# Kernel tuning notes

Hardware: AMD Instinct MI355X
Metric: run time of the kernel (lower is better)

Reference implementation:

```python
import jax, jax.numpy as jnp
import numpy as np

D_IN = 1024
D_OUT = 1024
NUM_HEADS = 16
HEAD_DIM = D_OUT // NUM_HEADS
EPS = 1e-6
POW = 16.0


def setup_inputs() -> dict:
    key = jax.random.key(0)
    ks = jax.random.split(key, 6)
    s = 1.0 / np.sqrt(D_IN)
    x = jax.random.normal(ks[0], (2, 2048, D_IN), dtype=jnp.float32)
    Wq = jax.random.uniform(ks[1], (D_OUT, D_IN), jnp.float32, -s, s)
    Wk = jax.random.uniform(ks[2], (D_OUT, D_IN), jnp.float32, -s, s)
    Wv = jax.random.uniform(ks[3], (D_OUT, D_IN), jnp.float32, -s, s)
    Wo = jax.random.uniform(ks[4], (D_OUT, D_OUT), jnp.float32, -s, s)
    bo = jax.random.uniform(ks[5], (D_OUT,), jnp.float32, -s, s)
    return {"x": x, "Wq": Wq, "Wk": Wk, "Wv": Wv, "Wo": Wo, "bo": bo}


def _l2norm(t):
    # torch F.normalize: t / max(||t||, eps)
    n = jnp.sqrt(jnp.sum(t * t, axis=-1, keepdims=True))
    return t / jnp.maximum(n, EPS)


def reference(x, Wq, Wk, Wv, Wo, bo):
    B, T, _ = x.shape
    # project and split heads: [B, H, T, Dh]
    def heads(W):
        y = jnp.einsum('btd,od->bto', x, W)
        return y.reshape(B, T, NUM_HEADS, HEAD_DIM).transpose(0, 2, 1, 3)
    Q = _l2norm(heads(Wq))
    K = _l2norm(heads(Wk))
    V = heads(Wv)
    cos_sim = jnp.clip(jnp.einsum('bhtd,bhsd->bhts', Q, K), -0.999, 0.999)
    scores = 1.0 - jnp.arccos(cos_sim) / jnp.pi
    W = jnp.power(jnp.maximum(scores, EPS), POW)
    W = W / (jnp.sum(W, axis=-1, keepdims=True) + EPS)
    out = jnp.einsum('bhts,bhsd->bhtd', W, V)
    out = out.transpose(0, 2, 1, 3).reshape(B, T, D_OUT)
    return jnp.einsum('bto,po->btp', out, Wo) + bo
```

## Files before the change

### kernel.cpp

```cpp
#include <hip/hip_runtime.h>
#include <math.h>

constexpr int Dm   = 1024;
constexpr int NH   = 16;
constexpr int HD   = 64;
constexpr int Bb   = 2;
constexpr int Tt   = 2048;
constexpr int MTOT = Bb * Tt;
#define EPSF 1e-6f

typedef __attribute__((ext_vector_type(8))) short short8;
typedef __attribute__((ext_vector_type(4))) float f32x4;
typedef __attribute__((ext_vector_type(2))) float f32x2;

__device__ __forceinline__ ushort f2bf(float f) {
    union { float f; unsigned u; } v; v.f = f;
    unsigned r = (v.u + 0x7FFFu + ((v.u >> 16) & 1u)) >> 16;
    return (ushort)r;
}

__device__ __forceinline__ void gload16(const void* g, void* l) {
    __builtin_amdgcn_global_load_lds(
        (const __attribute__((address_space(1))) unsigned int*)g,
        (__attribute__((address_space(3))) unsigned int*)l,
        16, 0, 0);
}

__global__ __launch_bounds__(256)
void cvt_all(const float* __restrict__ x,  const float* __restrict__ wq,
             const float* __restrict__ wk, const float* __restrict__ wv,
             const float* __restrict__ wo,
             ushort* __restrict__ xb,  ushort* __restrict__ wqb,
             ushort* __restrict__ wkb, ushort* __restrict__ wvb,
             ushort* __restrict__ wob) {
    int i = blockIdx.x * 256 + threadIdx.x;
    const float* src; ushort* dst; int off;
    if (i < 1048576)      { src = x;  dst = xb;  off = i; }
    else if (i < 1310720) { src = wq; dst = wqb; off = i - 1048576; }
    else if (i < 1572864) { src = wk; dst = wkb; off = i - 1310720; }
    else if (i < 1835008) { src = wv; dst = wvb; off = i - 1572864; }
    else                  { src = wo; dst = wob; off = i - 1835008; }
    const float4 v = ((const float4*)src)[off];
    ushort4 o;
    o.x = f2bf(v.x); o.y = f2bf(v.y); o.z = f2bf(v.z); o.w = f2bf(v.w);
    ((ushort4*)dst)[off] = o;
}

template<bool OUTF32>
__device__ __forceinline__
void gemm_core(const ushort* __restrict__ A, const ushort* __restrict__ W,
               const float* __restrict__ bias, void* __restrict__ out,
               int m0, int n0, int N, int K, int mode) {
    __shared__ ushort As[128 * 64];
    __shared__ ushort Bs[128 * 64];
    const int tid  = threadIdx.x;
    const int wave = tid >> 6, lane = tid & 63;
    const int quad = lane >> 4, l15 = lane & 15;
    const int wr = wave >> 1, wc = wave & 1;
    const int lr = lane >> 3;
    const int sc = (lane & 7) ^ lr;

    f32x4 acc[4][4] = {};
    const ushort* Ab = A + (size_t)(m0 + lr) * K + sc * 8;
    const ushort* Wb = W + (size_t)(n0 + lr) * K + sc * 8;

    for (int k0 = 0; k0 < K; k0 += 64) {
        #pragma unroll
        for (int i = 0; i < 4; i++) {
            const int rows8 = (wave * 4 + i) * 8;
            gload16(Ab + (size_t)rows8 * K + k0, &As[rows8 * 64]);
            gload16(Wb + (size_t)rows8 * K + k0, &Bs[rows8 * 64]);
        }
        __syncthreads();
        #pragma unroll
        for (int kh = 0; kh < 2; kh++) {
            short8 af[4];
            #pragma unroll
            for (int mi = 0; mi < 4; mi++) {
                const int row = wr * 64 + mi * 16 + l15;
                af[mi] = *(const short8*)&As[row * 64 + (((kh * 4 + quad) ^ (row & 7)) * 8)];
            }
            #pragma unroll
            for (int nj = 0; nj < 4; nj++) {
                const int row = wc * 64 + nj * 16 + l15;
                const short8 bf = *(const short8*)&Bs[row * 64 + (((kh * 4 + quad) ^ (row & 7)) * 8)];
                #pragma unroll
                for (int mi = 0; mi < 4; mi++)
                    acc[mi][nj] = __builtin_amdgcn_mfma_f32_16x16x32_bf16(af[mi], bf, acc[mi][nj], 0, 0, 0);
            }
        }
        __syncthreads();
    }

    if (!OUTF32 && mode == 2) {
        #pragma unroll
        for (int mi = 0; mi < 4; mi++) {
            const int t  = m0 + wr * 64 + mi * 16 + quad * 4;
            const int bb = t >> 11, tl = t & 2047;
            #pragma unroll
            for (int nj = 0; nj < 4; nj++) {
                const int n = n0 + wc * 64 + nj * 16 + l15;
                const int hh = n >> 6, dd = n & 63;
                uint2 pk;
                pk.x = (unsigned)f2bf(acc[mi][nj][0]) | ((unsigned)f2bf(acc[mi][nj][1]) << 16);
                pk.y = (unsigned)f2bf(acc[mi][nj][2]) | ((unsigned)f2bf(acc[mi][nj][3]) << 16);
                *(uint2*)&((ushort*)out)[(size_t)((bb * NH + hh) * HD + dd) * Tt + tl] = pk;
            }
        }
        return;
    }

    #pragma unroll
    for (int mi = 0; mi < 4; mi++) {
        float inv[4] = {1.f, 1.f, 1.f, 1.f};
        if (!OUTF32 && mode == 1) {
            #pragma unroll
            for (int r = 0; r < 4; r++) {
                float ss = 0.f;
                #pragma unroll
                for (int nj = 0; nj < 4; nj++) ss += acc[mi][nj][r] * acc[mi][nj][r];
                ss += __shfl_xor(ss, 1); ss += __shfl_xor(ss, 2);
                ss += __shfl_xor(ss, 4); ss += __shfl_xor(ss, 8);
                inv[r] = 1.f / fmaxf(sqrtf(ss), EPSF);
            }
        }
        #pragma unroll
        for (int nj = 0; nj < 4; nj++)
            #pragma unroll
            for (int r = 0; r < 4; r++) {
                const int row = m0 + wr * 64 + mi * 16 + quad * 4 + r;
                const int col = n0 + wc * 64 + nj * 16 + l15;
                if (OUTF32)
                    ((float*)out)[(size_t)row * N + col] = acc[mi][nj][r] + bias[col];
                else
                    ((ushort*)out)[(size_t)row * N + col] = f2bf(acc[mi][nj][r] * inv[r]);
            }
    }
}

__global__ __launch_bounds__(256)
void qkv_gemm(const ushort* __restrict__ xb,
              const ushort* __restrict__ wq, const ushort* __restrict__ wk,
              const ushort* __restrict__ wv,
              ushort* __restrict__ qb, ushort* __restrict__ kb,
              ushort* __restrict__ vtb) {
    const int ny = blockIdx.y, sel = ny >> 3;
    const ushort* W = (sel == 0) ? wq : (sel == 1) ? wk : wv;
    ushort* out     = (sel == 0) ? qb : (sel == 1) ? kb : vtb;
    gemm_core<false>(xb, W, nullptr, out, blockIdx.x * 128, (ny & 7) * 128,
                     Dm, Dm, (sel < 2) ? 1 : 2);
}

__global__ __launch_bounds__(256)
void out_gemm(const ushort* __restrict__ aob, const ushort* __restrict__ wob,
              const float* __restrict__ bias, float* __restrict__ out) {
    gemm_core<true>(aob, wob, bias, out, blockIdx.x * 128, blockIdx.y * 128,
                    Dm, Dm, 0);
}

__global__ __launch_bounds__(256)
void attn_kernel(const ushort* __restrict__ Qb, const ushort* __restrict__ Kb,
                 const ushort* __restrict__ Vtb, ushort* __restrict__ Ob) {
    __shared__ ushort Ks[2][64 * 64];
    __shared__ ushort Vs[2][64 * 64];
    __shared__ ushort Ws[64 * 64];
    const int tid  = threadIdx.x;
    const int wave = tid >> 6, lane = tid & 63;
    const int quad = lane >> 4, l15 = lane & 15;
    const int t0 = blockIdx.x * 64, h = blockIdx.y, b = blockIdx.z;

    const size_t qrow = (size_t)(b * Tt + t0 + 16 * wave + l15) * Dm + h * HD;
    const short8 qf0 = *(const short8*)&Qb[qrow + quad * 8];
    const short8 qf1 = *(const short8*)&Qb[qrow + 32 + quad * 8];

    const size_t kbase  = (size_t)(b * Tt) * Dm + h * HD;
    const size_t vtbase = (size_t)((b * NH + h) * HD) * Tt;
    const int r0 = tid >> 3, ch0 = tid & 7;
    const ushort* kg = Kb  + kbase  + (size_t)r0 * Dm + ch0 * 8;
    const ushort* vg = Vtb + vtbase + (size_t)r0 * Tt + ch0 * 8;
    const int lsw0 = r0 * 64 + ((ch0 ^ (r0 & 7)) * 8);
    const int lsw1 = (r0 + 32) * 64 + ((ch0 ^ (r0 & 7)) * 8);

    f32x4 oacc[4] = {};
    f32x2 denp[4] = {};

    const f32x2 k3 = {-0.00596162f, -0.00596162f};
    const f32x2 k2 = { 0.02363680f,  0.02363680f};
    const f32x2 k1 = {-0.06751768f, -0.06751768f};
    const f32x2 k0 = { 0.49997415f,  0.49997415f};

    short8 pk0 = *(const short8*)kg;
    short8 pk1 = *(const short8*)(kg + (size_t)32 * Dm);
    short8 pv0 = *(const short8*)vg;
    short8 pv1 = *(const short8*)(vg + (size_t)32 * Tt);
    *(short8*)&Ks[0][lsw0] = pk0;  *(short8*)&Ks[0][lsw1] = pk1;
    *(short8*)&Vs[0][lsw0] = pv0;  *(short8*)&Vs[0][lsw1] = pv1;
    __syncthreads();

    for (int i = 0; i < 32; i++) {
        const int p = i & 1;
        if (i < 31) {
            const size_t sn = (size_t)(i + 1) * 64;
            pk0 = *(const short8*)(kg + sn * Dm);
            pk1 = *(const short8*)(kg + (sn + 32) * Dm);
            pv0 = *(const short8*)(vg + sn);
            pv1 = *(const short8*)(vg + sn + (size_t)32 * Tt);
        }

        f32x4 sf[4] = {};
        #pragma unroll
        for (int j = 0; j < 4; j++) {
            const int row = 16 * j + l15;
            const short8 kf0 = *(const short8*)&Ks[p][row * 64 + ((quad ^ (row & 7)) * 8)];
            const short8 kf1 = *(const short8*)&Ks[p][row * 64 + (((4 + quad) ^ (row & 7)) * 8)];
            sf[j] = __builtin_amdgcn_mfma_f32_16x16x32_bf16(qf0, kf0, sf[j], 0, 0, 0);
            sf[j] = __builtin_amdgcn_mfma_f32_16x16x32_bf16(qf1, kf1, sf[j], 0, 0, 0);
        }

        #pragma unroll
        for (int r = 0; r < 4; r++) {
            f32x2 ca, cb;
            ca.x = __builtin_amdgcn_fmed3f(sf[0][r], -0.999f, 0.999f);
            ca.y = __builtin_amdgcn_fmed3f(sf[1][r], -0.999f, 0.999f);
            cb.x = __builtin_amdgcn_fmed3f(sf[2][r], -0.999f, 0.999f);
            cb.y = __builtin_amdgcn_fmed3f(sf[3][r], -0.999f, 0.999f);
            f32x2 axa = {fabsf(ca.x), fabsf(ca.y)};
            f32x2 axb = {fabsf(cb.x), fabsf(cb.y)};
            f32x2 pa = __builtin_elementwise_fma(axa, k3, k2);
            f32x2 pb = __builtin_elementwise_fma(axb, k3, k2);
            pa = __builtin_elementwise_fma(pa, axa, k1);
            pb = __builtin_elementwise_fma(pb, axb, k1);
            pa = __builtin_elementwise_fma(pa, axa, k0);
            pb = __builtin_elementwise_fma(pb, axb, k0);
            f32x2 ta = 1.0f - axa, tb = 1.0f - axb;
            ta.x = __builtin_amdgcn_sqrtf(ta.x); ta.y = __builtin_amdgcn_sqrtf(ta.y);
            tb.x = __builtin_amdgcn_sqrtf(tb.x); tb.y = __builtin_amdgcn_sqrtf(tb.y);
            const f32x2 rpa = ta * pa, rpb = tb * pb;
            const f32x2 da = 0.5f - rpa, db = 0.5f - rpb;
            f32x2 csa = {__builtin_copysignf(da.x, ca.x), __builtin_copysignf(da.y, ca.y)};
            f32x2 csb = {__builtin_copysignf(db.x, cb.x), __builtin_copysignf(db.y, cb.y)};
            f32x2 wa = csa + 0.5f, wb = csb + 0.5f;
            wa *= wa; wa *= wa; wa *= wa; wa *= wa;
            wb *= wb; wb *= wb; wb *= wb; wb *= wb;
            denp[r] += wa; denp[r] += wb;
            const int wrow = 16 * wave + quad * 4 + r;
            const int wb7 = wrow & 7;
            const int base = wrow * 64 + (l15 & 7);
            const int hc = l15 >> 3;
            Ws[base + (((hc)     ^ wb7) * 8)] = f2bf(wa.x);
            Ws[base + (((hc + 2) ^ wb7) * 8)] = f2bf(wa.y);
            Ws[base + (((hc + 4) ^ wb7) * 8)] = f2bf(wb.x);
            Ws[base + (((hc + 6) ^ wb7) * 8)] = f2bf(wb.y);
        }
        __syncthreads();

        const int wrow = 16 * wave + l15;
        const short8 wf0 = *(const short8*)&Ws[wrow * 64 + ((quad ^ (wrow & 7)) * 8)];
        const short8 wf1 = *(const short8*)&Ws[wrow * 64 + (((4 + quad) ^ (wrow & 7)) * 8)];
        #pragma unroll
        for (int j = 0; j < 4; j++) {
            const int vrow = 16 * j + l15;
            const short8 vf0 = *(const short8*)&Vs[p][vrow * 64 + ((quad ^ (vrow & 7)) * 8)];
            const short8 vf1 = *(const short8*)&Vs[p][vrow * 64 + (((4 + quad) ^ (vrow & 7)) * 8)];
            oacc[j] = __builtin_amdgcn_mfma_f32_16x16x32_bf16(wf0, vf0, oacc[j], 0, 0, 0);
            oacc[j] = __builtin_amdgcn_mfma_f32_16x16x32_bf16(wf1, vf1, oacc[j], 0, 0, 0);
        }
        if (i < 31) {
            *(short8*)&Ks[1 - p][lsw0] = pk0;  *(short8*)&Ks[1 - p][lsw1] = pk1;
            *(short8*)&Vs[1 - p][lsw0] = pv0;  *(short8*)&Vs[1 - p][lsw1] = pv1;
        }
        __syncthreads();
    }

    float den[4];
    #pragma unroll
    for (int r = 0; r < 4; r++) {
        float d = denp[r].x + denp[r].y;
        d += __shfl_xor(d, 1); d += __shfl_xor(d, 2);
        d += __shfl_xor(d, 4); d += __shfl_xor(d, 8);
        den[r] = d;
    }
    const size_t obase =
        (size_t)(b * Tt + t0 + 16 * wave + quad * 4) * Dm + h * HD + l15;
    #pragma unroll
    for (int j = 0; j < 4; j++)
        #pragma unroll
        for (int r = 0; r < 4; r++)
            Ob[obase + (size_t)r * Dm + 16 * j] = f2bf(oacc[j][r] / (den[r] + EPSF));
}

extern "C" void kernel_launch(void* const* d_in, const int* in_sizes, int n_in,
                              void* d_out, int out_size, void* d_ws, size_t ws_size,
                              hipStream_t stream) {
    const float* x  = (const float*)d_in[0];
    const float* Wq = (const float*)d_in[1];
    const float* Wk = (const float*)d_in[2];
    const float* Wv = (const float*)d_in[3];
    const float* Wo = (const float*)d_in[4];
    const float* bo = (const float*)d_in[5];
    float* out = (float*)d_out;

    ushort* ws = (ushort*)d_ws;
    const size_t M1 = 1u << 20;
    ushort* xb  = ws;
    ushort* wqb = ws + 4 * M1;
    ushort* wkb = ws + 5 * M1;
    ushort* wvb = ws + 6 * M1;
    ushort* wob = ws + 7 * M1;
    ushort* qb  = ws + 8 * M1;
    ushort* kb  = ws + 12 * M1;
    ushort* vtb = ws + 16 * M1;
    ushort* aob = ws + 20 * M1;

    cvt_all<<<8192, 256, 0, stream>>>(x, Wq, Wk, Wv, Wo, xb, wqb, wkb, wvb, wob);
    qkv_gemm<<<dim3(MTOT / 128, 24), 256, 0, stream>>>(xb, wqb, wkb, wvb, qb, kb, vtb);
    attn_kernel<<<dim3(Tt / 64, NH, Bb), 256, 0, stream>>>(qb, kb, vtb, aob);
    out_gemm<<<dim3(MTOT / 128, Dm / 128), 256, 0, stream>>>(aob, wob, bo, out);
}
```

Before: 236.4 us.

## Simplify arccos weight polynomial, cheaper bf16 rounding, reciprocal normalize, smaller out-GEMM tiles

Rewrites the attention weight computation to fit 1 - acos(c)/pi directly as sqrt(1-c) times a cubic in (1-c). This removes the abs, copysign and extra subtract steps from the hot elementwise loop. P values are now rounded to bf16 by simple round-half-up instead of round-to-nearest-even, and the final normalization uses one reciprocal per row instead of a divide per element. The output GEMM becomes a dedicated 64x128-tile kernel with twice as many blocks, for better CU occupancy on 256 CUs. The changes carry some accuracy risk from the new polynomial fit and rounding mode.

```diff
diff --git a/kernel.cpp b/kernel.cpp
--- a/kernel.cpp
+++ b/kernel.cpp
@@ -17,6 +17,9 @@
     union { float f; unsigned u; } v; v.f = f;
     unsigned r = (v.u + 0x7FFFu + ((v.u >> 16) & 1u)) >> 16;
     return (ushort)r;
+}
+__device__ __forceinline__ ushort f2bf_hu(float f) {
+    return (ushort)((__builtin_bit_cast(unsigned, f) + 0x8000u) >> 16);
 }
 
 __device__ __forceinline__ void gload16(const void* g, void* l) {
@@ -152,10 +155,64 @@
 }
 
 __global__ __launch_bounds__(256)
-void out_gemm(const ushort* __restrict__ aob, const ushort* __restrict__ wob,
+void out_gemm(const ushort* __restrict__ A, const ushort* __restrict__ W,
               const float* __restrict__ bias, float* __restrict__ out) {
-    gemm_core<true>(aob, wob, bias, out, blockIdx.x * 128, blockIdx.y * 128,
-                    Dm, Dm, 0);
+    __shared__ ushort As[64 * 64];
+    __shared__ ushort Bs[128 * 64];
+    const int tid  = threadIdx.x;
+    const int wave = tid >> 6, lane = tid & 63;
+    const int quad = lane >> 4, l15 = lane & 15;
+    const int wm = wave & 1, wn = wave >> 1;
+    const int lr = lane >> 3;
+    const int sc = (lane & 7) ^ lr;
+    const int m0 = blockIdx.x * 64, n0 = blockIdx.y * 128;
+    const int K = Dm, N = Dm;
+
+    f32x4 acc[2][4] = {};
+    const ushort* Ab = A + (size_t)(m0 + lr) * K + sc * 8;
+    const ushort* Wb = W + (size_t)(n0 + lr) * K + sc * 8;
+
+    for (int k0 = 0; k0 < K; k0 += 64) {
+        #pragma unroll
+        for (int i = 0; i < 2; i++) {
+            const int rows8 = (wave * 2 + i) * 8;
+            gload16(Ab + (size_t)rows8 * K + k0, &As[rows8 * 64]);
+        }
+        #pragma unroll
+        for (int i = 0; i < 4; i++) {
+            const int rows8 = (wave * 4 + i) * 8;
+            gload16(Wb + (size_t)rows8 * K + k0, &Bs[rows8 * 64]);
+        }
+        __syncthreads();
+        #pragma unroll
+        for (int kh = 0; kh < 2; kh++) {
+            short8 af[2];
+            #pragma unroll
+            for (int mi = 0; mi < 2; mi++) {
+                const int row = wm * 32 + mi * 16 + l15;
+                af[mi] = *(const short8*)&As[row * 64 + (((kh * 4 + quad) ^ (row & 7)) * 8)];
+            }
+            #pragma unroll
+            for (int nj = 0; nj < 4; nj++) {
+                const int row = wn * 64 + nj * 16 + l15;
+                const short8 bf = *(const short8*)&Bs[row * 64 + (((kh * 4 + quad) ^ (row & 7)) * 8)];
+                #pragma unroll
+                for (int mi = 0; mi < 2; mi++)
+                    acc[mi][nj] = __builtin_amdgcn_mfma_f32_16x16x32_bf16(af[mi], bf, acc[mi][nj], 0, 0, 0);
+            }
+        }
+        __syncthreads();
+    }
+    #pragma unroll
+    for (int mi = 0; mi < 2; mi++)
+        #pragma unroll
+        for (int nj = 0; nj < 4; nj++)
+            #pragma unroll
+            for (int r = 0; r < 4; r++) {
+                const int row = m0 + wm * 32 + mi * 16 + quad * 4 + r;
+                const int col = n0 + wn * 64 + nj * 16 + l15;
+                out[(size_t)row * N + col] = acc[mi][nj][r] + bias[col];
+            }
 }
 
 __global__ __launch_bounds__(256)
@@ -184,10 +241,10 @@
     f32x4 oacc[4] = {};
     f32x2 denp[4] = {};
 
-    const f32x2 k3 = {-0.00596162f, -0.00596162f};
-    const f32x2 k2 = { 0.02363680f,  0.02363680f};
-    const f32x2 k1 = {-0.06751768f, -0.06751768f};
-    const f32x2 k0 = { 0.49997415f,  0.49997415f};
+    const f32x2 h3 = { 0.011180f,  0.011180f};
+    const f32x2 h2 = {-0.002070f, -0.002070f};
+    const f32x2 h1 = { 0.040732f,  0.040732f};
+    const f32x2 h0 = { 0.450158f,  0.450158f};
 
     short8 pk0 = *(const short8*)kg;
     short8 pk1 = *(const short8*)(kg + (size_t)32 * Dm);
@@ -219,27 +276,23 @@
 
         #pragma unroll
         for (int r = 0; r < 4; r++) {
-            f32x2 ca, cb;
-            ca.x = __builtin_amdgcn_fmed3f(sf[0][r], -0.999f, 0.999f);
-            ca.y = __builtin_amdgcn_fmed3f(sf[1][r], -0.999f, 0.999f);
-            cb.x = __builtin_amdgcn_fmed3f(sf[2][r], -0.999f, 0.999f);
-            cb.y = __builtin_amdgcn_fmed3f(sf[3][r], -0.999f, 0.999f);
-            f32x2 axa = {fabsf(ca.x), fabsf(ca.y)};
-            f32x2 axb = {fabsf(cb.x), fabsf(cb.y)};
-            f32x2 pa = __builtin_elementwise_fma(axa, k3, k2);
-            f32x2 pb = __builtin_elementwise_fma(axb, k3, k2);
-            pa = __builtin_elementwise_fma(pa, axa, k1);
-            pb = __builtin_elementwise_fma(pb, axb, k1);
-            pa = __builtin_elementwise_fma(pa, axa, k0);
-            pb = __builtin_elementwise_fma(pb, axb, k0);
-            f32x2 ta = 1.0f - axa, tb = 1.0f - axb;
-            ta.x = __builtin_amdgcn_sqrtf(ta.x); ta.y = __builtin_amdgcn_sqrtf(ta.y);
-            tb.x = __builtin_amdgcn_sqrtf(tb.x); tb.y = __builtin_amdgcn_sqrtf(tb.y);
-            const f32x2 rpa = ta * pa, rpb = tb * pb;
-            const f32x2 da = 0.5f - rpa, db = 0.5f - rpb;
-            f32x2 csa = {__builtin_copysignf(da.x, ca.x), __builtin_copysignf(da.y, ca.y)};
-            f32x2 csb = {__builtin_copysignf(db.x, cb.x), __builtin_copysignf(db.y, cb.y)};
-            f32x2 wa = csa + 0.5f, wb = csb + 0.5f;
+            f32x2 tA, tB;
+            tA.x = __builtin_amdgcn_fmed3f(1.0f - sf[0][r], 0.001f, 1.999f);
+            tA.y = __builtin_amdgcn_fmed3f(1.0f - sf[1][r], 0.001f, 1.999f);
+            tB.x = __builtin_amdgcn_fmed3f(1.0f - sf[2][r], 0.001f, 1.999f);
+            tB.y = __builtin_amdgcn_fmed3f(1.0f - sf[3][r], 0.001f, 1.999f);
+            f32x2 pa = __builtin_elementwise_fma(tA, h3, h2);
+            f32x2 pb = __builtin_elementwise_fma(tB, h3, h2);
+            pa = __builtin_elementwise_fma(pa, tA, h1);
+            pb = __builtin_elementwise_fma(pb, tB, h1);
+            pa = __builtin_elementwise_fma(pa, tA, h0);
+            pb = __builtin_elementwise_fma(pb, tB, h0);
+            f32x2 ra, rb;
+            ra.x = __builtin_amdgcn_sqrtf(tA.x); ra.y = __builtin_amdgcn_sqrtf(tA.y);
+            rb.x = __builtin_amdgcn_sqrtf(tB.x); rb.y = __builtin_amdgcn_sqrtf(tB.y);
+            const f32x2 one2 = {1.0f, 1.0f};
+            f32x2 wa = __builtin_elementwise_fma(-ra, pa, one2);
+            f32x2 wb = __builtin_elementwise_fma(-rb, pb, one2);
             wa *= wa; wa *= wa; wa *= wa; wa *= wa;
             wb *= wb; wb *= wb; wb *= wb; wb *= wb;
             denp[r] += wa; denp[r] += wb;
@@ -247,10 +300,10 @@
             const int wb7 = wrow & 7;
             const int base = wrow * 64 + (l15 & 7);
             const int hc = l15 >> 3;
-            Ws[base + (((hc)     ^ wb7) * 8)] = f2bf(wa.x);
-            Ws[base + (((hc + 2) ^ wb7) * 8)] = f2bf(wa.y);
-            Ws[base + (((hc + 4) ^ wb7) * 8)] = f2bf(wb.x);
-            Ws[base + (((hc + 6) ^ wb7) * 8)] = f2bf(wb.y);
+            Ws[base + (((hc)     ^ wb7) * 8)] = f2bf_hu(wa.x);
+            Ws[base + (((hc + 2) ^ wb7) * 8)] = f2bf_hu(wa.y);
+            Ws[base + (((hc + 4) ^ wb7) * 8)] = f2bf_hu(wb.x);
+            Ws[base + (((hc + 6) ^ wb7) * 8)] = f2bf_hu(wb.y);
         }
         __syncthreads();
 
@@ -278,7 +331,7 @@
         float d = denp[r].x + denp[r].y;
         d += __shfl_xor(d, 1); d += __shfl_xor(d, 2);
         d += __shfl_xor(d, 4); d += __shfl_xor(d, 8);
-        den[r] = d;
+        den[r] = __builtin_amdgcn_rcpf(d + EPSF);
     }
     const size_t obase =
         (size_t)(b * Tt + t0 + 16 * wave + quad * 4) * Dm + h * HD + l15;
@@ -286,7 +339,7 @@
     for (int j = 0; j < 4; j++)
         #pragma unroll
         for (int r = 0; r < 4; r++)
-            Ob[obase + (size_t)r * Dm + 16 * j] = f2bf(oacc[j][r] / (den[r] + EPSF));
+            Ob[obase + (size_t)r * Dm + 16 * j] = f2bf(oacc[j][r] * den[r]);
 }
 
 extern "C" void kernel_launch(void* const* d_in, const int* in_sizes, int n_in,
@@ -315,5 +368,5 @@
     cvt_all<<<8192, 256, 0, stream>>>(x, Wq, Wk, Wv, Wo, xb, wqb, wkb, wvb, wob);
     qkv_gemm<<<dim3(MTOT / 128, 24), 256, 0, stream>>>(xb, wqb, wkb, wvb, qb, kb, vtb);
     attn_kernel<<<dim3(Tt / 64, NH, Bb), 256, 0, stream>>>(qb, kb, vtb, aob);
-    out_gemm<<<dim3(MTOT / 128, Dm / 128), 256, 0, stream>>>(aob, wob, bo, out);
-}
+    out_gemm<<<dim3(MTOT / 64, Dm / 128), 256, 0, stream>>>(aob, wob, bo, out);
+}
```

New measurement: 225.4 us. -4.7%, faster.
